# Performance work log

Hardware: AMD Instinct MI355X
Metric: run time of the kernel (lower is better)

Reference implementation:

```python
import jax, jax.numpy as jnp
import numpy as np
from jax import lax

K = 5          # CARAFE kernel size
STRIDE = 2     # scale_factor (downsample)
ENC_PAD = 1    # (encoder_kernel-1)*dilation/2 = 1


def conv2d(x, w, b, stride, padding):
    out = lax.conv_general_dilated(
        x, w, (stride, stride), [(padding, padding), (padding, padding)],
        dimension_numbers=('NCHW', 'OIHW', 'NCHW'))
    return out + b[None, :, None, None]


def setup_inputs() -> dict:
    key = jax.random.key(0)
    ks = jax.random.split(key, 4)
    B, C, H, W = 4, 256, 128, 128
    CC = 64
    x = jax.random.normal(ks[0], (B, C, H, W), dtype=jnp.float32)
    w_comp = jax.random.normal(ks[1], (CC, C, 1, 1), dtype=jnp.float32) * (1.0 / np.sqrt(C))
    b_comp = jnp.zeros((CC,), jnp.float32)
    w_enc = jax.random.normal(ks[2], (K * K, CC, 3, 3), dtype=jnp.float32) * (1.0 / np.sqrt(CC * 9))
    b_enc = jnp.zeros((K * K,), jnp.float32)
    w_kenc = jax.random.normal(ks[3], (16, CC, 3, 3), dtype=jnp.float32) * (1.0 / np.sqrt(CC * 9))
    b_kenc = jnp.zeros((16,), jnp.float32)
    return {'x': x, 'w_comp': w_comp, 'b_comp': b_comp,
            'w_enc': w_enc, 'b_enc': b_enc,
            'w_kenc': w_kenc, 'b_kenc': b_kenc}


def reference(x, w_comp, b_comp, w_enc, b_enc, w_kenc, b_kenc):
    B, C, H, W = x.shape
    # channel compressor (1x1 conv)
    cx = conv2d(x, w_comp, b_comp, stride=1, padding=0)          # (B,CC,H,W)
    # content encoder -> mask logits at downsampled grid
    mask = conv2d(cx, w_enc, b_enc, stride=STRIDE, padding=ENC_PAD)   # (B,K*K,Ho,Wo)
    # kernel encoder -> per-pixel temperature via channel product (Power/PI)
    ke = conv2d(cx, w_kenc, b_kenc, stride=STRIDE, padding=ENC_PAD)   # (B,16,Ho,Wo)
    i = jnp.clip(jnp.prod(ke, axis=1, keepdims=True), -10.0, 10.0)    # (B,1,Ho,Wo)
    mask = mask * i
    Ho, Wo = mask.shape[2], mask.shape[3]
    # softmax over the K*K kernel positions (group=1)
    mask = jax.nn.softmax(mask.reshape(B, 1, K * K, Ho, Wo), axis=2)
    mask = mask.reshape(B, K * K, Ho, Wo)
    # feature reassembly: unfold + weighted sum over kernel window
    pad = K // 2
    patches = lax.conv_general_dilated_patches(
        x, filter_shape=(K, K), window_strides=(STRIDE, STRIDE),
        padding=[(pad, pad), (pad, pad)],
        dimension_numbers=('NCHW', 'OIHW', 'NCHW'))                   # (B, C*K*K, Ho, Wo)
    patches = patches.reshape(B, C, K * K, Ho, Wo)
    out = jnp.einsum('bckhw,bkhw->bchw', patches, mask)
    return out
```

## Files before the change

### kernel.cpp

```cpp
#include <hip/hip_runtime.h>

#define H_IN   128
#define W_IN   128
#define HW_IN  16384
#define C_IN   256
#define CC     64
#define HO     64
#define WO     64
#define HWO    4096
#define NB     4
#define NPX    16384
#define NCHP   48
#define NPH    16

#define OFF_WC    0
#define OFF_WE    16384
#define OFF_CX    44032
#define OFF_PART  4238336
#define OFF_MASK  16821248
#define OFF_RED   17230848

__global__ __launch_bounds__(256) void prep_kernel(
    const float* __restrict__ wc, const float* __restrict__ we,
    const float* __restrict__ wk, float* __restrict__ ws) {
  int i = blockIdx.x * 256 + threadIdx.x;
  if (i < 16384) {
    int ccg = i >> 11, c = (i >> 3) & 255, j = i & 7;
    ws[OFF_WC + i] = wc[(ccg * 8 + j) * C_IN + c];
  } else if (i < 44032) {
    int e = i - 16384;
    int row = e / 48, ch = e - row * 48;
    float v = 0.f;
    if (ch < 25)      v = we[ch * 576 + row];
    else if (ch < 41) v = wk[(ch - 25) * 576 + row];
    ws[OFF_WE + e] = v;
  }
}

__global__ __launch_bounds__(1024) void compress_kernel(
    const float* __restrict__ x, const float* __restrict__ bcomp,
    const float* __restrict__ wsr, float* __restrict__ cx) {
  __shared__ float red[8][64][33];
  int tid = threadIdx.x;
  int wv = tid >> 6, lane = tid & 63;
  int ccg = __builtin_amdgcn_readfirstlane(wv & 7);
  int kh  = __builtin_amdgcn_readfirstlane(wv >> 3);
  int gq = blockIdx.x * 64 + lane;
  int b = gq >> 12;
  int p = (gq & 4095) << 2;
  const float* xb = x + (size_t)b * C_IN * HW_IN + p;
  const float* wp = wsr + OFF_WC + ccg * (256 * 8);
  float4 acc[8];
#pragma unroll
  for (int j = 0; j < 8; ++j) acc[j] = make_float4(0.f, 0.f, 0.f, 0.f);
  int cbase = kh * 128;
  float4 xv[4], xn[4];
#pragma unroll
  for (int u = 0; u < 4; ++u)
    xv[u] = *(const float4*)(xb + (size_t)(cbase + u) * HW_IN);
  for (int c0 = 0; c0 < 128; c0 += 4) {
    if (c0 + 4 < 128) {
#pragma unroll
      for (int u = 0; u < 4; ++u)
        xn[u] = *(const float4*)(xb + (size_t)(cbase + c0 + 4 + u) * HW_IN);
    }
#pragma unroll
    for (int u = 0; u < 4; ++u) {
      const float* wrow = wp + (cbase + c0 + u) * 8;
      float4 xu = xv[u];
#pragma unroll
      for (int j = 0; j < 8; ++j) {
        float wj = wrow[j];
        acc[j].x = fmaf(wj, xu.x, acc[j].x);
        acc[j].y = fmaf(wj, xu.y, acc[j].y);
        acc[j].z = fmaf(wj, xu.z, acc[j].z);
        acc[j].w = fmaf(wj, xu.w, acc[j].w);
      }
    }
#pragma unroll
    for (int u = 0; u < 4; ++u) xv[u] = xn[u];
  }
  if (kh == 1) {
    float* d = &red[ccg][lane][0];
#pragma unroll
    for (int j = 0; j < 8; ++j) {
      d[j * 4 + 0] = acc[j].x; d[j * 4 + 1] = acc[j].y;
      d[j * 4 + 2] = acc[j].z; d[j * 4 + 3] = acc[j].w;
    }
  }
  __syncthreads();
  if (kh == 0) {
    const float* d = &red[ccg][lane][0];
#pragma unroll
    for (int j = 0; j < 8; ++j) {
      int cc = ccg * 8 + j;
      float bj = bcomp[cc];
      float4 o;
      o.x = acc[j].x + d[j * 4 + 0] + bj;
      o.y = acc[j].y + d[j * 4 + 1] + bj;
      o.z = acc[j].z + d[j * 4 + 2] + bj;
      o.w = acc[j].w + d[j * 4 + 3] + bj;
      *(float4*)(cx + ((size_t)b * CC + cc) * HW_IN + p) = o;
    }
  }
}

__global__ __launch_bounds__(256) void encoder_kernel(
    const float* __restrict__ wsr, float* __restrict__ part) {
  __shared__ float lds[4][9][136];
  const float* cx   = wsr + OFF_CX;
  const float* wall = wsr + OFF_WE;
  int gb = blockIdx.x;
  int hog = gb & 15, b = (gb >> 4) & 3, ph = gb >> 6;
  int tid = threadIdx.x;
  int ci0 = ph * 4;
  int hi0 = hog * 8 - 1;

  for (int i = tid; i < 144; i += 256) {
    int ci = i / 36; int r = (i % 36) >> 2; int j = i & 3;
    lds[ci][r][j] = 0.f;
  }
  for (int i = tid; i < 1152; i += 256) {
    int ci = i / 288; int r2 = i - ci * 288;
    int row = r2 >> 5, c4 = r2 & 31;
    int hi = hi0 + row;
    float4 v = make_float4(0.f, 0.f, 0.f, 0.f);
    if ((unsigned)hi < 128u)
      v = *(const float4*)(cx + ((size_t)(b * CC + ci0 + ci) * HW_IN) + hi * W_IN + c4 * 4);
    *(float4*)(&lds[ci][row][4 + c4 * 4]) = v;
  }
  __syncthreads();

  int wo = tid & 63, hs = tid >> 6;
  float acc[41];
#pragma unroll
  for (int ch = 0; ch < 41; ++ch) acc[ch] = 0.f;
  const float* lp = &lds[0][2 * hs][3 + 2 * wo];
#pragma unroll
  for (int ci = 0; ci < 4; ++ci) {
#pragma unroll
    for (int k3 = 0; k3 < 3; ++k3) {
#pragma unroll
      for (int kw = 0; kw < 3; ++kw) {
        float v = lp[ci * 1224 + k3 * 136 + kw];
        const float* w = wall + ((ci0 + ci) * 9 + k3 * 3 + kw) * 48;
#pragma unroll
        for (int ch = 0; ch < 41; ++ch) acc[ch] = fmaf(w[ch], v, acc[ch]);
      }
    }
  }
  int px = b * HWO + (hog * 4 + hs) * 64 + wo;
  float* pb = part + (size_t)ph * NCHP * NPX + px;
#pragma unroll
  for (int ch = 0; ch < 41; ++ch) pb[(size_t)ch * NPX] = acc[ch];
}

__global__ __launch_bounds__(256) void reduce_kernel(
    const float* __restrict__ wsr, float* __restrict__ red) {
  const float* part = wsr + OFF_PART;
  int i = blockIdx.x * 256 + threadIdx.x;
  int ch = i >> 12, p4 = i & 4095;
  size_t off = (size_t)ch * NPX + p4 * 4;
  float4 s = make_float4(0.f, 0.f, 0.f, 0.f);
#pragma unroll
  for (int ph = 0; ph < NPH; ++ph) {
    float4 v = *(const float4*)(part + (size_t)ph * NCHP * NPX + off);
    s.x += v.x; s.y += v.y; s.z += v.z; s.w += v.w;
  }
  *(float4*)(red + off) = s;
}

__global__ __launch_bounds__(64) void softmax_kernel(
    const float* __restrict__ wsr, const float* __restrict__ benc,
    const float* __restrict__ bkenc, float* __restrict__ mask) {
  const float* red = wsr + OFF_RED;
  int px = blockIdx.x * 64 + threadIdx.x;
  float lg[41];
#pragma unroll
  for (int ch = 0; ch < 41; ++ch) {
    float b = (ch < 25) ? benc[ch] : bkenc[ch - 25];
    lg[ch] = b + red[(size_t)ch * NPX + px];
  }
  float prod = lg[25];
#pragma unroll
  for (int ch = 26; ch < 41; ++ch) prod *= lg[ch];
  float iv = fminf(fmaxf(prod, -10.f), 10.f);
  float m = -1e30f;
#pragma unroll
  for (int ch = 0; ch < 25; ++ch) { lg[ch] *= iv; m = fmaxf(m, lg[ch]); }
  float sum = 0.f;
#pragma unroll
  for (int ch = 0; ch < 25; ++ch) { lg[ch] = __expf(lg[ch] - m); sum += lg[ch]; }
  float inv = 1.0f / sum;
#pragma unroll
  for (int ch = 0; ch < 25; ++ch)
    mask[(size_t)ch * NPX + px] = lg[ch] * inv;
}

__global__ __launch_bounds__(256) void reassemble_kernel(
    const float* __restrict__ x, const float* __restrict__ wsr,
    float* __restrict__ out) {
  __shared__ float lds[4][11][136];
  const float* mask = wsr + OFF_MASK;
  int tid = threadIdx.x;
  int gb = blockIdx.x;
  int cg = gb & 63, hog = (gb >> 6) & 15, b = gb >> 10;
  int hi0 = hog * 8 - 2;

  for (int i = tid; i < 352; i += 256) {
    int ch = i / 88; int r = i - ch * 88; int row = r >> 3; int p = r & 7;
    int idx = (p < 4) ? p : (128 + p);
    lds[ch][row][idx] = 0.f;
  }
  for (int i = tid; i < 1408; i += 256) {
    int ch = i / 352; int r = i - ch * 352;
    int row = r >> 5, c4 = r & 31;
    int hi = hi0 + row;
    float4 v = make_float4(0.f, 0.f, 0.f, 0.f);
    if ((unsigned)hi < 128u) {
      int c = cg * 4 + ch;
      v = *(const float4*)(x + ((size_t)(b * C_IN + c) * HW_IN) + hi * W_IN + c4 * 4);
    }
    *(float4*)(&lds[ch][row][4 + c4 * 4]) = v;
  }
  __syncthreads();

  int wo = tid & 63, hs = tid >> 6;
  int ho = hog * 4 + hs;
  int opix = ho * WO + wo;
  int gpx = b * HWO + opix;
  float mk[25];
#pragma unroll
  for (int k = 0; k < 25; ++k)
    mk[k] = mask[(size_t)k * NPX + gpx];
#pragma unroll
  for (int ch = 0; ch < 4; ++ch) {
    const float* lp = &lds[ch][2 * hs][2 + 2 * wo];
    float s = 0.f;
#pragma unroll
    for (int kh = 0; kh < 5; ++kh)
#pragma unroll
      for (int kw = 0; kw < 5; ++kw)
        s = fmaf(mk[kh * 5 + kw], lp[kh * 136 + kw], s);
    int c = cg * 4 + ch;
    out[(size_t)(b * C_IN + c) * HWO + opix] = s;
  }
}

extern "C" void kernel_launch(void* const* d_in, const int* in_sizes, int n_in,
                              void* d_out, int out_size, void* d_ws, size_t ws_size,
                              hipStream_t stream) {
  const float* x      = (const float*)d_in[0];
  const float* w_comp = (const float*)d_in[1];
  const float* b_comp = (const float*)d_in[2];
  const float* w_enc  = (const float*)d_in[3];
  const float* b_enc  = (const float*)d_in[4];
  const float* w_kenc = (const float*)d_in[5];
  const float* b_kenc = (const float*)d_in[6];
  float* ws  = (float*)d_ws;
  float* out = (float*)d_out;

  prep_kernel<<<172, 256, 0, stream>>>(w_comp, w_enc, w_kenc, ws);
  compress_kernel<<<256, 1024, 0, stream>>>(x, b_comp, ws, ws + OFF_CX);
  encoder_kernel<<<1024, 256, 0, stream>>>(ws, ws + OFF_PART);
  reduce_kernel<<<656, 256, 0, stream>>>(ws, ws + OFF_RED);
  softmax_kernel<<<256, 64, 0, stream>>>(ws, b_enc, b_kenc, ws + OFF_MASK);
  reassemble_kernel<<<4096, 256, 0, stream>>>(x, ws, out);
}
```

Measured before the change: 184.9 us.

## Fold weight prep into compress kernel and split output channels across blocks

Removes the separate prep kernel launch. The encoder weight transposition now runs inside the first 54 threads of each compress block, and the 1x1 compression weights are read directly from the original layout instead of a pre-transposed copy. The compress kernel now launches 512 blocks of 512 threads, each covering half the output channels, which doubles the block count but makes each block read x twice overall. Channel loads are double-buffered in two groups of four. The encoder kernel reads the transposed weights written by compress, which relies on stream ordering.

```diff
diff --git a/kernel.cpp b/kernel.cpp
--- a/kernel.cpp
+++ b/kernel.cpp
@@ -13,72 +13,81 @@
 #define NCHP   48
 #define NPH    16
 
-#define OFF_WC    0
 #define OFF_WE    16384
 #define OFF_CX    44032
 #define OFF_PART  4238336
 #define OFF_MASK  16821248
 #define OFF_RED   17230848
 
-__global__ __launch_bounds__(256) void prep_kernel(
-    const float* __restrict__ wc, const float* __restrict__ we,
+__global__ __launch_bounds__(512) void compress_kernel(
+    const float* __restrict__ x, const float* __restrict__ wc,
+    const float* __restrict__ bcomp, const float* __restrict__ we,
     const float* __restrict__ wk, float* __restrict__ ws) {
-  int i = blockIdx.x * 256 + threadIdx.x;
-  if (i < 16384) {
-    int ccg = i >> 11, c = (i >> 3) & 255, j = i & 7;
-    ws[OFF_WC + i] = wc[(ccg * 8 + j) * C_IN + c];
-  } else if (i < 44032) {
-    int e = i - 16384;
+  int gb = blockIdx.x, tid = threadIdx.x;
+  if (tid < 54) {
+    int e = gb * 54 + tid;
     int row = e / 48, ch = e - row * 48;
     float v = 0.f;
     if (ch < 25)      v = we[ch * 576 + row];
     else if (ch < 41) v = wk[(ch - 25) * 576 + row];
     ws[OFF_WE + e] = v;
   }
-}
-
-__global__ __launch_bounds__(1024) void compress_kernel(
-    const float* __restrict__ x, const float* __restrict__ bcomp,
-    const float* __restrict__ wsr, float* __restrict__ cx) {
-  __shared__ float red[8][64][33];
-  int tid = threadIdx.x;
+  __shared__ float red[4][64][33];
   int wv = tid >> 6, lane = tid & 63;
-  int ccg = __builtin_amdgcn_readfirstlane(wv & 7);
-  int kh  = __builtin_amdgcn_readfirstlane(wv >> 3);
-  int gq = blockIdx.x * 64 + lane;
-  int b = gq >> 12;
-  int p = (gq & 4095) << 2;
+  int ccg = __builtin_amdgcn_readfirstlane(wv & 3);
+  int kh  = __builtin_amdgcn_readfirstlane(wv >> 2);
+  int ccw = gb & 1;
+  int pxb = gb >> 1;
+  int b = pxb >> 6;
+  int p = (pxb & 63) * 256 + lane * 4;
+  int cc0 = ccw * 32 + ccg * 8;
   const float* xb = x + (size_t)b * C_IN * HW_IN + p;
-  const float* wp = wsr + OFF_WC + ccg * (256 * 8);
+  int cbase = kh * 128;
   float4 acc[8];
 #pragma unroll
   for (int j = 0; j < 8; ++j) acc[j] = make_float4(0.f, 0.f, 0.f, 0.f);
-  int cbase = kh * 128;
-  float4 xv[4], xn[4];
+  float4 xa[4], xc[4];
 #pragma unroll
   for (int u = 0; u < 4; ++u)
-    xv[u] = *(const float4*)(xb + (size_t)(cbase + u) * HW_IN);
-  for (int c0 = 0; c0 < 128; c0 += 4) {
-    if (c0 + 4 < 128) {
-#pragma unroll
-      for (int u = 0; u < 4; ++u)
-        xn[u] = *(const float4*)(xb + (size_t)(cbase + c0 + 4 + u) * HW_IN);
-    }
+    xa[u] = *(const float4*)(xb + (size_t)(cbase + u) * HW_IN);
+#pragma unroll
+  for (int u = 0; u < 4; ++u)
+    xc[u] = *(const float4*)(xb + (size_t)(cbase + 4 + u) * HW_IN);
+  for (int c0 = 0; c0 < 128; c0 += 8) {
 #pragma unroll
     for (int u = 0; u < 4; ++u) {
-      const float* wrow = wp + (cbase + c0 + u) * 8;
-      float4 xu = xv[u];
+      float4 xu = xa[u];
 #pragma unroll
       for (int j = 0; j < 8; ++j) {
-        float wj = wrow[j];
+        float wj = wc[(size_t)(cc0 + j) * C_IN + cbase + c0 + u];
         acc[j].x = fmaf(wj, xu.x, acc[j].x);
         acc[j].y = fmaf(wj, xu.y, acc[j].y);
         acc[j].z = fmaf(wj, xu.z, acc[j].z);
         acc[j].w = fmaf(wj, xu.w, acc[j].w);
       }
     }
-#pragma unroll
-    for (int u = 0; u < 4; ++u) xv[u] = xn[u];
+    if (c0 + 8 < 128) {
+#pragma unroll
+      for (int u = 0; u < 4; ++u)
+        xa[u] = *(const float4*)(xb + (size_t)(cbase + c0 + 8 + u) * HW_IN);
+    }
+#pragma unroll
+    for (int u = 0; u < 4; ++u) {
+      float4 xu = xc[u];
+#pragma unroll
+      for (int j = 0; j < 8; ++j) {
+        float wj = wc[(size_t)(cc0 + j) * C_IN + cbase + c0 + 4 + u];
+        acc[j].x = fmaf(wj, xu.x, acc[j].x);
+        acc[j].y = fmaf(wj, xu.y, acc[j].y);
+        acc[j].z = fmaf(wj, xu.z, acc[j].z);
+        acc[j].w = fmaf(wj, xu.w, acc[j].w);
+      }
+    }
+    if (c0 + 12 < 128) {
+#pragma unroll
+      for (int u = 0; u < 4; ++u)
+        xc[u] = *(const float4*)(xb + (size_t)(cbase + c0 + 12 + u) * HW_IN);
+    }
   }
   if (kh == 1) {
     float* d = &red[ccg][lane][0];
@@ -90,10 +99,11 @@
   }
   __syncthreads();
   if (kh == 0) {
+    float* cx = ws + OFF_CX;
     const float* d = &red[ccg][lane][0];
 #pragma unroll
     for (int j = 0; j < 8; ++j) {
-      int cc = ccg * 8 + j;
+      int cc = cc0 + j;
       float bj = bcomp[cc];
       float4 o;
       o.x = acc[j].x + d[j * 4 + 0] + bj;
@@ -260,8 +270,7 @@
   float* ws  = (float*)d_ws;
   float* out = (float*)d_out;
 
-  prep_kernel<<<172, 256, 0, stream>>>(w_comp, w_enc, w_kenc, ws);
-  compress_kernel<<<256, 1024, 0, stream>>>(x, b_comp, ws, ws + OFF_CX);
+  compress_kernel<<<512, 512, 0, stream>>>(x, w_comp, b_comp, w_enc, w_kenc, ws);
   encoder_kernel<<<1024, 256, 0, stream>>>(ws, ws + OFF_PART);
   reduce_kernel<<<656, 256, 0, stream>>>(ws, ws + OFF_RED);
   softmax_kernel<<<256, 64, 0, stream>>>(ws, b_enc, b_kenc, ws + OFF_MASK);
```

Measured after the change: 182.5 us. About the same (-1.3%).
